# Performance work log

Measured on AMD Instinct MI355X. Metric: run time of the kernel, lower is better.

The kernel has to match this reference:

```python
import jax, jax.numpy as jnp
import numpy as np

B, L, H = 2, 1024, 768
DI, N, K, R = 1536, 16, 4, 48


def setup_inputs() -> dict:
    key = jax.random.key(0)
    ks = jax.random.split(key, 10)
    s = 0.02
    inp = {
        "x": jax.random.normal(ks[0], (B, L, H), jnp.float32),
        "in_up_w": jax.random.normal(ks[1], (2 * DI * 4, H), jnp.float32) * s,
        "in_down_w": jax.random.normal(ks[2], (2 * DI, 2 * DI * 4), jnp.float32) * s,
        "conv_w": jax.random.normal(ks[3], (DI, 1, K), jnp.float32) * 0.5,
        "conv_b": jnp.zeros((DI,), jnp.float32),
        "x_proj_w": jax.random.normal(ks[4], (R + 2 * N, DI), jnp.float32) * s,
        "dt_w": jax.random.normal(ks[5], (DI, R), jnp.float32) * s,
        "dt_b": jnp.full((DI,), -4.0, jnp.float32) + jax.random.normal(ks[6], (DI,), jnp.float32) * 0.1,
        "A_log": jnp.log(jnp.broadcast_to(jnp.arange(1, N + 1, dtype=jnp.float32)[None, :], (DI, N))),
        "D": jnp.ones((DI,), jnp.float32),
        "out_up_w": jax.random.normal(ks[7], (4 * DI, DI), jnp.float32) * s,
        "out_down_w": jax.random.normal(ks[8], (H, 4 * DI), jnp.float32) * s,
    }
    return inp


def reference(x, in_up_w, in_down_w, conv_w, conv_b, x_proj_w, dt_w, dt_b,
              A_log, D, out_up_w, out_down_w):
    act = jax.nn.silu
    # in_up_proj -> act -> in_down_proj  (use_bias=False)
    proj = act(x @ in_up_w.T) @ in_down_w.T          # [B, L, 2*DI]
    proj = proj.transpose(0, 2, 1)                   # [B, 2*DI, L]
    hs, gate = jnp.split(proj, 2, axis=1)            # each [B, DI, L]

    # depthwise causal conv1d (pad left K-1, truncate to L) + SiLU
    k = conv_w.shape[-1]
    c = hs.shape[1]
    y = jax.lax.conv_general_dilated(
        hs, conv_w, window_strides=(1,), padding=[(k - 1, 0)],
        feature_group_count=c, dimension_numbers=("NCH", "OIH", "NCH"))
    hs = act(y + conv_b[None, :, None])              # [B, DI, L]

    # x_proj -> split into dt / B / C
    ssm_p = jnp.einsum("bdl,kd->blk", hs, x_proj_w)  # [B, L, R+2N]
    r = dt_w.shape[1]
    n = A_log.shape[1]
    ts, Bm, Cm = jnp.split(ssm_p, [r, r + n], axis=-1)
    dt = jax.nn.softplus(ts @ dt_w.T + dt_b)         # [B, L, DI]
    dt = dt.transpose(0, 2, 1)                       # [B, DI, L]

    A = -jnp.exp(A_log)                              # [DI, N]
    dA = jnp.exp(dt[..., None] * A[None, :, None, :])        # [B, DI, L, N]
    dBu = dt[..., None] * Bm[:, None, :, :] * hs[..., None]  # [B, DI, L, N]

    def step(s, inps):
        dA_t, dBu_t, C_t = inps          # [B,DI,N], [B,DI,N], [B,N]
        s = dA_t * s + dBu_t
        return s, jnp.einsum("bdn,bn->bd", s, C_t)

    s0 = jnp.zeros((x.shape[0], c, n), x.dtype)
    _, ys = jax.lax.scan(
        step, s0,
        (dA.transpose(2, 0, 1, 3), dBu.transpose(2, 0, 1, 3), Cm.transpose(1, 0, 2)))
    yscan = ys.transpose(1, 2, 0)                    # [B, DI, L]

    yscan = yscan + hs * D[None, :, None]
    yscan = yscan * act(gate)

    # out_up_proj -> act -> out_down_proj (use_bias=False)
    out = act(yscan.transpose(0, 2, 1) @ out_up_w.T) @ out_down_w.T  # [B, L, H]
    return out
```

## Files before the change

### kernel.cpp

```cpp
#include <hip/hip_runtime.h>
#include <hip/hip_bf16.h>
#include <cstdint>

#define B_   2
#define L_   1024
#define H_   768
#define DI_  1536
#define DI2_ 3072
#define DUP_ 12288
#define DOUT_ 6144
#define N_   16
#define R_   48
#define SPW  128
#define BL_  2048
#define C_   64
#define CL_  16

typedef __bf16 bf16x8 __attribute__((ext_vector_type(8)));
typedef float  f32x4  __attribute__((ext_vector_type(4)));
typedef unsigned int u32;

__device__ __forceinline__ float silu_f(float v) {
    return v / (1.f + __expf(-v));
}

__device__ __forceinline__ void async_ld16(const void* g, void* lds) {
    __builtin_amdgcn_global_load_lds(
        (const __attribute__((address_space(1))) u32*)g,
        (__attribute__((address_space(3))) u32*)lds, 16, 0, 0);
}

__device__ __forceinline__ void cvt8(const float* __restrict__ s, __bf16* __restrict__ d, int i)
{
    const float4 a = *(const float4*)(s + i);
    const float4 b = *(const float4*)(s + i + 4);
    bf16x8 v;
    v[0] = (__bf16)a.x; v[1] = (__bf16)a.y; v[2] = (__bf16)a.z; v[3] = (__bf16)a.w;
    v[4] = (__bf16)b.x; v[5] = (__bf16)b.y; v[6] = (__bf16)b.z; v[7] = (__bf16)b.w;
    *(bf16x8*)(d + i) = v;
}

__global__ void prep1(const float* __restrict__ x, const float* __restrict__ wup,
                      const float* __restrict__ wdn,
                      __bf16* __restrict__ xb, __bf16* __restrict__ wupb,
                      __bf16* __restrict__ wdnb)
{
    const int bid = blockIdx.x;
    if (bid < 768)            cvt8(x,   xb,   (bid * 256 + threadIdx.x) * 8);
    else if (bid < 5376)      cvt8(wup, wupb, ((bid - 768) * 256 + threadIdx.x) * 8);
    else                      cvt8(wdn, wdnb, ((bid - 5376) * 256 + threadIdx.x) * 8);
}

__global__ void prep2(const float* __restrict__ woup, const float* __restrict__ wodn,
                      const float* __restrict__ xp, const float* __restrict__ dtw,
                      __bf16* __restrict__ woupb, __bf16* __restrict__ wodnb,
                      __bf16* __restrict__ xppad, float* __restrict__ dtwT)
{
    const int bid = blockIdx.x;
    if (bid < 4608)        cvt8(woup, woupb, (bid * 256 + threadIdx.x) * 8);
    else if (bid < 6912)   cvt8(wodn, wodnb, ((bid - 4608) * 256 + threadIdx.x) * 8);
    else if (bid < 7008) {
        const int i = ((bid - 6912) * 256 + threadIdx.x) * 8;
        const int j = i / DI_;
        bf16x8 v;
        if (j < 80) {
            const float4 a = *(const float4*)(xp + i);
            const float4 b = *(const float4*)(xp + i + 4);
            v[0] = (__bf16)a.x; v[1] = (__bf16)a.y; v[2] = (__bf16)a.z; v[3] = (__bf16)a.w;
            v[4] = (__bf16)b.x; v[5] = (__bf16)b.y; v[6] = (__bf16)b.z; v[7] = (__bf16)b.w;
        } else {
            for (int k = 0; k < 8; ++k) v[k] = (__bf16)0.f;
        }
        *(bf16x8*)(xppad + i) = v;
    } else {
        const int i = (bid - 7008) * 256 + threadIdx.x;
        const int r = i / DI_, d = i % DI_;
        dtwT[i] = dtw[(size_t)d * R_ + r];
    }
}

template<int EPI, int ATOMIC, typename OutT>
__global__ __launch_bounds__(256) void gemm_bf16(
    const __bf16* __restrict__ A, const __bf16* __restrict__ W, OutT* __restrict__ O,
    int M, int N, int Kslice, int lda, int ldw, int ldo)
{
    constexpr int BM = 128, BN = 128, BK = 32;
    __shared__ __bf16 As[BM * BK];
    __shared__ __bf16 Bs[BN * BK];

    const int tid  = threadIdx.x;
    const int bm   = blockIdx.x * BM;
    const int bn   = blockIdx.y * BN;
    const int kbase = blockIdx.z * Kslice;
    if (ATOMIC == 0) O += (size_t)blockIdx.z * (size_t)M * ldo;

    const int wave = tid >> 6, lane = tid & 63;
    const int wm = (wave >> 1) * 64, wn = (wave & 1) * 64;
    const int quad = lane >> 4, tr = lane & 15;

    const int srow = tid >> 2;
    const int skc  = ((tid & 3) ^ ((srow >> 1) & 3)) * 8;
    const __bf16* Ag0 = A + (size_t)(bm + srow) * lda + kbase + skc;
    const __bf16* Ag1 = A + (size_t)(bm + srow + 64) * lda + kbase + skc;
    const __bf16* Wg0 = W + (size_t)(bn + srow) * ldw + kbase + skc;
    const __bf16* Wg1 = W + (size_t)(bn + srow + 64) * ldw + kbase + skc;
    __bf16* Al0 = &As[tid * 8];
    __bf16* Al1 = &As[2048 + tid * 8];
    __bf16* Bl0 = &Bs[tid * 8];
    __bf16* Bl1 = &Bs[2048 + tid * 8];

    const int fsw = (quad ^ ((tr >> 1) & 3)) * 8;
    const __bf16* arp = &As[(wm + tr) * BK + fsw];
    const __bf16* brp = &Bs[(wn + tr) * BK + fsw];

    f32x4 acc[4][4];
#pragma unroll
    for (int i = 0; i < 4; ++i)
#pragma unroll
        for (int j = 0; j < 4; ++j) acc[i][j] = (f32x4){0.f, 0.f, 0.f, 0.f};

    for (int k0 = 0; k0 < Kslice; k0 += BK) {
        __syncthreads();
        async_ld16(Ag0 + k0, Al0);
        async_ld16(Ag1 + k0, Al1);
        async_ld16(Wg0 + k0, Bl0);
        async_ld16(Wg1 + k0, Bl1);
        __syncthreads();

        bf16x8 af[4], bfv[4];
#pragma unroll
        for (int i = 0; i < 4; ++i) af[i]  = *(const bf16x8*)(arp + i * 16 * BK);
#pragma unroll
        for (int j = 0; j < 4; ++j) bfv[j] = *(const bf16x8*)(brp + j * 16 * BK);
#pragma unroll
        for (int i = 0; i < 4; ++i)
#pragma unroll
            for (int j = 0; j < 4; ++j)
                acc[i][j] = __builtin_amdgcn_mfma_f32_16x16x32_bf16(af[i], bfv[j], acc[i][j], 0, 0, 0);
    }

#pragma unroll
    for (int i = 0; i < 4; ++i) {
        const int row = bm + wm + i * 16 + quad * 4;
#pragma unroll
        for (int j = 0; j < 4; ++j) {
            const int col = bn + wn + j * 16 + tr;
            OutT* op = O + (size_t)row * ldo + col;
#pragma unroll
            for (int r = 0; r < 4; ++r) {
                float v = acc[i][j][r];
                if (EPI == 1) v = silu_f(v);
                if (ATOMIC == 1) atomicAdd((float*)(op + (size_t)r * ldo), v);
                else             op[(size_t)r * ldo] = (OutT)v;
            }
        }
    }
}

__global__ void conv_kernel(const float* __restrict__ P0, const float* __restrict__ P1,
                            const float* __restrict__ cw, const float* __restrict__ cb,
                            float* __restrict__ HS, __bf16* __restrict__ HSb)
{
    const int t = blockIdx.x * blockDim.x + threadIdx.x;
    const int d = t % DI_;
    const int bl = t / DI_;
    const int l = bl % L_;
    const float4 w = *(const float4*)(cw + (size_t)d * 4);
    const float wk[4] = {w.x, w.y, w.z, w.w};
    float acc = cb[d];
#pragma unroll
    for (int k = 0; k < 4; ++k) {
        const int ls = l - 3 + k;
        if (ls >= 0) {
            const size_t idx = (size_t)(bl - l + ls) * DI2_ + d;
            acc += wk[k] * (P0[idx] + P1[idx]);
        }
    }
    const float h = silu_f(acc);
    HS[t]  = h;
    HSb[t] = (__bf16)h;
}

__global__ void dt_kernel(const float* __restrict__ SP, const float* __restrict__ dtwT,
                          const float* __restrict__ dtb, float* __restrict__ DT)
{
    const int t = blockIdx.x * blockDim.x + threadIdx.x;
    const int d = t % DI_;
    const int bl = t / DI_;
    const float* ts = SP + (size_t)bl * SPW;
    float s = dtb[d];
#pragma unroll
    for (int r4 = 0; r4 < R_ / 4; ++r4) {
        const float4 tv = *(const float4*)(ts + r4 * 4);
        const float* wp = dtwT + (size_t)r4 * 4 * DI_ + d;
        s += tv.x * wp[0] + tv.y * wp[DI_] + tv.z * wp[2 * DI_] + tv.w * wp[3 * DI_];
    }
    DT[t] = (s > 20.f) ? s : log1pf(__expf(s));
}

__global__ __launch_bounds__(256) void scan_pass1(
    const float* __restrict__ DT, const float* __restrict__ HS,
    const float* __restrict__ SP, const float* __restrict__ A_log,
    float* __restrict__ Aprod, float* __restrict__ Bacc)
{
    const int t = blockIdx.x * blockDim.x + threadIdx.x;
    const int d = t % DI_;
    const int y = t / DI_;
    const int c = y % C_;
    const int b = y / C_;
    float A[N_], s[N_], ap[N_];
    {
        const float4* alp = (const float4*)(A_log + (size_t)d * N_);
        const float4 a0 = alp[0], a1 = alp[1], a2 = alp[2], a3 = alp[3];
        const float av[N_] = {a0.x,a0.y,a0.z,a0.w, a1.x,a1.y,a1.z,a1.w,
                              a2.x,a2.y,a2.z,a2.w, a3.x,a3.y,a3.z,a3.w};
#pragma unroll
        for (int n = 0; n < N_; ++n) { A[n] = -__expf(av[n]); s[n] = 0.f; ap[n] = 1.f; }
    }
    for (int il = 0; il < CL_; ++il) {
        const size_t bl = (size_t)b * L_ + c * CL_ + il;
        const float dt = DT[bl * DI_ + d];
        const float hs = HS[bl * DI_ + d];
        const float4* Bp = (const float4*)(SP + bl * SPW + R_);
        const float4 b0 = Bp[0], b1 = Bp[1], b2 = Bp[2], b3 = Bp[3];
        const float Bv[N_] = {b0.x,b0.y,b0.z,b0.w, b1.x,b1.y,b1.z,b1.w,
                              b2.x,b2.y,b2.z,b2.w, b3.x,b3.y,b3.z,b3.w};
        const float dh = dt * hs;
#pragma unroll
        for (int n = 0; n < N_; ++n) {
            const float dA = __expf(dt * A[n]);
            s[n] = fmaf(dA, s[n], dh * Bv[n]);
            ap[n] *= dA;
        }
    }
    float4* Ap = (float4*)(Aprod + (size_t)t * N_);
    float4* Bc = (float4*)(Bacc  + (size_t)t * N_);
    Ap[0] = make_float4(ap[0], ap[1], ap[2], ap[3]);
    Ap[1] = make_float4(ap[4], ap[5], ap[6], ap[7]);
    Ap[2] = make_float4(ap[8], ap[9], ap[10], ap[11]);
    Ap[3] = make_float4(ap[12], ap[13], ap[14], ap[15]);
    Bc[0] = make_float4(s[0], s[1], s[2], s[3]);
    Bc[1] = make_float4(s[4], s[5], s[6], s[7]);
    Bc[2] = make_float4(s[8], s[9], s[10], s[11]);
    Bc[3] = make_float4(s[12], s[13], s[14], s[15]);
}

__global__ __launch_bounds__(256) void scan_pass2(
    const float* __restrict__ Aprod, const float* __restrict__ Bacc,
    float* __restrict__ Sinit)
{
    const int t = blockIdx.x * blockDim.x + threadIdx.x;
    const int n = t & (N_ - 1);
    const int d = (t >> 4) % DI_;
    const int b = (t >> 4) / DI_;
    float s = 0.f;
    for (int c = 0; c < C_; ++c) {
        const size_t idx = (((size_t)b * C_ + c) * DI_ + d) * N_ + n;
        Sinit[idx] = s;
        s = fmaf(Aprod[idx], s, Bacc[idx]);
    }
}

__global__ __launch_bounds__(256) void scan_pass3(
    const float* __restrict__ DT, const float* __restrict__ HS,
    const float* __restrict__ SP, const float* __restrict__ P0,
    const float* __restrict__ P1, const float* __restrict__ A_log,
    const float* __restrict__ Dv, const float* __restrict__ Sinit,
    __bf16* __restrict__ Y)
{
    const int t = blockIdx.x * blockDim.x + threadIdx.x;
    const int d = t % DI_;
    const int y = t / DI_;
    const int c = y % C_;
    const int b = y / C_;
    float A[N_], s[N_];
    {
        const float4* alp = (const float4*)(A_log + (size_t)d * N_);
        const float4 a0 = alp[0], a1 = alp[1], a2 = alp[2], a3 = alp[3];
        const float av[N_] = {a0.x,a0.y,a0.z,a0.w, a1.x,a1.y,a1.z,a1.w,
                              a2.x,a2.y,a2.z,a2.w, a3.x,a3.y,a3.z,a3.w};
#pragma unroll
        for (int n = 0; n < N_; ++n) A[n] = -__expf(av[n]);
    }
    {
        const float4* sp = (const float4*)(Sinit + (size_t)t * N_);
        const float4 s0 = sp[0], s1 = sp[1], s2 = sp[2], s3 = sp[3];
        s[0]=s0.x; s[1]=s0.y; s[2]=s0.z; s[3]=s0.w;
        s[4]=s1.x; s[5]=s1.y; s[6]=s1.z; s[7]=s1.w;
        s[8]=s2.x; s[9]=s2.y; s[10]=s2.z; s[11]=s2.w;
        s[12]=s3.x; s[13]=s3.y; s[14]=s3.z; s[15]=s3.w;
    }
    const float Dd = Dv[d];
    for (int il = 0; il < CL_; ++il) {
        const size_t bl = (size_t)b * L_ + c * CL_ + il;
        const float dt = DT[bl * DI_ + d];
        const float hs = HS[bl * DI_ + d];
        const float4* Bp = (const float4*)(SP + bl * SPW + R_);
        const float4 b0 = Bp[0], b1 = Bp[1], b2 = Bp[2], b3 = Bp[3];
        const float4 c0 = Bp[4], c1 = Bp[5], c2 = Bp[6], c3 = Bp[7];
        const float Bv[N_] = {b0.x,b0.y,b0.z,b0.w, b1.x,b1.y,b1.z,b1.w,
                              b2.x,b2.y,b2.z,b2.w, b3.x,b3.y,b3.z,b3.w};
        const float Cv[N_] = {c0.x,c0.y,c0.z,c0.w, c1.x,c1.y,c1.z,c1.w,
                              c2.x,c2.y,c2.z,c2.w, c3.x,c3.y,c3.z,c3.w};
        const float dh = dt * hs;
        float acc = 0.f;
#pragma unroll
        for (int n = 0; n < N_; ++n) {
            const float dA = __expf(dt * A[n]);
            s[n] = fmaf(dA, s[n], dh * Bv[n]);
            acc = fmaf(s[n], Cv[n], acc);
        }
        const size_t gidx = bl * DI2_ + DI_ + d;
        const float g = P0[gidx] + P1[gidx];
        Y[bl * DI_ + d] = (__bf16)((acc + hs * Dd) * silu_f(g));
    }
}

extern "C" void kernel_launch(void* const* d_in, const int* in_sizes, int n_in,
                              void* d_out, int out_size, void* d_ws, size_t ws_size,
                              hipStream_t stream) {
    const float* x        = (const float*)d_in[0];
    const float* w_up     = (const float*)d_in[1];
    const float* w_down   = (const float*)d_in[2];
    const float* conv_w   = (const float*)d_in[3];
    const float* conv_b   = (const float*)d_in[4];
    const float* x_proj_w = (const float*)d_in[5];
    const float* dt_w     = (const float*)d_in[6];
    const float* dt_b     = (const float*)d_in[7];
    const float* A_log    = (const float*)d_in[8];
    const float* Dvec     = (const float*)d_in[9];
    const float* w_oup    = (const float*)d_in[10];
    const float* w_odown  = (const float*)d_in[11];
    float* out = (float*)d_out;

    char* base = (char*)d_ws;
    __bf16* x_b      = (__bf16*)base;
    __bf16* wup_b    = (__bf16*)(base + 3145728);
    float*  P0       = (float*)base;
    float*  P1       = (float*)(base + 25165824);
    char* r2 = base + 50331648;
    __bf16* wdown_b  = (__bf16*)r2;
    __bf16* HSb      = (__bf16*)r2;
    float*  SPb      = (float*)(r2 + 6291456);
    float*  DTb      = (float*)(r2 + 7340032);
    __bf16* Yb       = (__bf16*)(r2 + 19922944);
    __bf16* XPpad    = (__bf16*)(r2 + 26214400);
    float*  dtwT     = (float*)(r2 + 26607616);
    __bf16* woup_b   = (__bf16*)(r2 + 26902528);
    __bf16* wodown_b = (__bf16*)(r2 + 45776896);
    char* r3 = r2 + 75497472;
    __bf16* U1b      = (__bf16*)r3;
    __bf16* U2b      = (__bf16*)r3;
    float*  Aprod    = (float*)r3;
    float*  Bacc     = (float*)(r3 + 12582912);
    float*  Sinit    = (float*)(r3 + 25165824);
    float*  HS       = (float*)(r3 + 37748736);

    prep1<<<23808, 256, 0, stream>>>(x, w_up, w_down, x_b, wup_b, wdown_b);

    gemm_bf16<1, 0, __bf16><<<dim3(16, 96, 1), 256, 0, stream>>>(
        x_b, wup_b, U1b, BL_, DUP_, H_, H_, H_, DUP_);

    gemm_bf16<0, 0, float><<<dim3(16, 24, 2), 256, 0, stream>>>(
        U1b, wdown_b, P0, BL_, DI2_, DUP_ / 2, DUP_, DUP_, DI2_);

    prep2<<<7296, 256, 0, stream>>>(w_oup, w_odown, x_proj_w, dt_w,
                                    woup_b, wodown_b, XPpad, dtwT);

    conv_kernel<<<(BL_ * DI_) / 256, 256, 0, stream>>>(P0, P1, conv_w, conv_b, HS, HSb);

    hipMemsetAsync(SPb, 0, (size_t)BL_ * SPW * 4, stream);
    gemm_bf16<0, 1, float><<<dim3(16, 1, 4), 256, 0, stream>>>(
        HSb, XPpad, SPb, BL_, SPW, DI_ / 4, DI_, DI_, SPW);

    dt_kernel<<<(BL_ * DI_) / 256, 256, 0, stream>>>(SPb, dtwT, dt_b, DTb);

    scan_pass1<<<(B_ * C_ * DI_) / 256, 256, 0, stream>>>(DTb, HS, SPb, A_log, Aprod, Bacc);
    scan_pass2<<<(B_ * DI_ * N_) / 256, 256, 0, stream>>>(Aprod, Bacc, Sinit);
    scan_pass3<<<(B_ * C_ * DI_) / 256, 256, 0, stream>>>(
        DTb, HS, SPb, P0, P1, A_log, Dvec, Sinit, Yb);

    gemm_bf16<1, 0, __bf16><<<dim3(16, 48, 1), 256, 0, stream>>>(
        Yb, woup_b, U2b, BL_, DOUT_, DI_, DI_, DI_, DOUT_);

    hipMemsetAsync(out, 0, (size_t)BL_ * H_ * 4, stream);
    gemm_bf16<0, 1, float><<<dim3(16, 6, 8), 256, 0, stream>>>(
        U2b, wodown_b, out, BL_, H_, DOUT_ / 8, DOUT_, DOUT_, H_);
}
```

Measured before the change: 825.2 us.

## Replace atomic split-K with partial buffers and reductions, swizzle blocks, drop fp32 HS

The two atomic split-K GEMMs (x_proj and out_down) now write per-slice partial outputs, which small reduce kernels then sum. This removes the memsets and the atomic traffic. The x_proj split grows from 4 to 8 slices and out_down shrinks from 8 to 4. The down-projection GEMM gets a block-index swizzle to improve cache locality. The fp32 copy of the conv output is dropped, so the scan passes read the bf16 version instead, cutting memory traffic at a small cost in precision.

```diff
diff --git a/kernel.cpp b/kernel.cpp
--- a/kernel.cpp
+++ b/kernel.cpp
@@ -79,7 +79,7 @@
     }
 }
 
-template<int EPI, int ATOMIC, typename OutT>
+template<int EPI, int ATOMIC, int SWZ, typename OutT>
 __global__ __launch_bounds__(256) void gemm_bf16(
     const __bf16* __restrict__ A, const __bf16* __restrict__ W, OutT* __restrict__ O,
     int M, int N, int Kslice, int lda, int ldw, int ldo)
@@ -89,8 +89,16 @@
     __shared__ __bf16 Bs[BN * BK];
 
     const int tid  = threadIdx.x;
-    const int bm   = blockIdx.x * BM;
-    const int bn   = blockIdx.y * BN;
+    int bx = blockIdx.x, by = blockIdx.y;
+    if (SWZ) {
+        const int nxy  = gridDim.x * gridDim.y;
+        const int flat = blockIdx.x + gridDim.x * blockIdx.y;
+        const int qq   = nxy >> 3;
+        const int s    = (flat & 7) * qq + (flat >> 3);
+        bx = s % gridDim.x; by = s / gridDim.x;
+    }
+    const int bm   = bx * BM;
+    const int bn   = by * BN;
     const int kbase = blockIdx.z * Kslice;
     if (ATOMIC == 0) O += (size_t)blockIdx.z * (size_t)M * ldo;
 
@@ -157,9 +165,33 @@
     }
 }
 
+__global__ void reduce_sp(const float* __restrict__ SPp, float* __restrict__ SPb)
+{
+    const int i = (blockIdx.x * 256 + threadIdx.x) * 4;
+    float4 a = *(const float4*)(SPp + i);
+#pragma unroll
+    for (int z = 1; z < 8; ++z) {
+        const float4 b = *(const float4*)(SPp + (size_t)z * (BL_ * SPW) + i);
+        a.x += b.x; a.y += b.y; a.z += b.z; a.w += b.w;
+    }
+    *(float4*)(SPb + i) = a;
+}
+
+__global__ void reduce_out(const float* __restrict__ OP, float* __restrict__ out)
+{
+    const int i = (blockIdx.x * 256 + threadIdx.x) * 4;
+    float4 a = *(const float4*)(OP + i);
+#pragma unroll
+    for (int z = 1; z < 4; ++z) {
+        const float4 b = *(const float4*)(OP + (size_t)z * (BL_ * H_) + i);
+        a.x += b.x; a.y += b.y; a.z += b.z; a.w += b.w;
+    }
+    *(float4*)(out + i) = a;
+}
+
 __global__ void conv_kernel(const float* __restrict__ P0, const float* __restrict__ P1,
                             const float* __restrict__ cw, const float* __restrict__ cb,
-                            float* __restrict__ HS, __bf16* __restrict__ HSb)
+                            __bf16* __restrict__ HSb)
 {
     const int t = blockIdx.x * blockDim.x + threadIdx.x;
     const int d = t % DI_;
@@ -176,9 +208,7 @@
             acc += wk[k] * (P0[idx] + P1[idx]);
         }
     }
-    const float h = silu_f(acc);
-    HS[t]  = h;
-    HSb[t] = (__bf16)h;
+    HSb[t] = (__bf16)silu_f(acc);
 }
 
 __global__ void dt_kernel(const float* __restrict__ SP, const float* __restrict__ dtwT,
@@ -199,7 +229,7 @@
 }
 
 __global__ __launch_bounds__(256) void scan_pass1(
-    const float* __restrict__ DT, const float* __restrict__ HS,
+    const float* __restrict__ DT, const __bf16* __restrict__ HSb,
     const float* __restrict__ SP, const float* __restrict__ A_log,
     float* __restrict__ Aprod, float* __restrict__ Bacc)
 {
@@ -220,7 +250,7 @@
     for (int il = 0; il < CL_; ++il) {
         const size_t bl = (size_t)b * L_ + c * CL_ + il;
         const float dt = DT[bl * DI_ + d];
-        const float hs = HS[bl * DI_ + d];
+        const float hs = (float)HSb[bl * DI_ + d];
         const float4* Bp = (const float4*)(SP + bl * SPW + R_);
         const float4 b0 = Bp[0], b1 = Bp[1], b2 = Bp[2], b3 = Bp[3];
         const float Bv[N_] = {b0.x,b0.y,b0.z,b0.w, b1.x,b1.y,b1.z,b1.w,
@@ -262,7 +292,7 @@
 }
 
 __global__ __launch_bounds__(256) void scan_pass3(
-    const float* __restrict__ DT, const float* __restrict__ HS,
+    const float* __restrict__ DT, const __bf16* __restrict__ HSb,
     const float* __restrict__ SP, const float* __restrict__ P0,
     const float* __restrict__ P1, const float* __restrict__ A_log,
     const float* __restrict__ Dv, const float* __restrict__ Sinit,
@@ -294,7 +324,7 @@
     for (int il = 0; il < CL_; ++il) {
         const size_t bl = (size_t)b * L_ + c * CL_ + il;
         const float dt = DT[bl * DI_ + d];
-        const float hs = HS[bl * DI_ + d];
+        const float hs = (float)HSb[bl * DI_ + d];
         const float4* Bp = (const float4*)(SP + bl * SPW + R_);
         const float4 b0 = Bp[0], b1 = Bp[1], b2 = Bp[2], b3 = Bp[3];
         const float4 c0 = Bp[4], c1 = Bp[5], c2 = Bp[6], c3 = Bp[7];
@@ -342,48 +372,49 @@
     __bf16* wdown_b  = (__bf16*)r2;
     __bf16* HSb      = (__bf16*)r2;
     float*  SPb      = (float*)(r2 + 6291456);
-    float*  DTb      = (float*)(r2 + 7340032);
-    __bf16* Yb       = (__bf16*)(r2 + 19922944);
-    __bf16* XPpad    = (__bf16*)(r2 + 26214400);
-    float*  dtwT     = (float*)(r2 + 26607616);
-    __bf16* woup_b   = (__bf16*)(r2 + 26902528);
-    __bf16* wodown_b = (__bf16*)(r2 + 45776896);
+    float*  SPp      = (float*)(r2 + 7340032);
+    float*  DTb      = (float*)(r2 + 15728640);
+    __bf16* Yb       = (__bf16*)(r2 + 28311552);
+    __bf16* XPpad    = (__bf16*)(r2 + 34603008);
+    float*  dtwT     = (float*)(r2 + 34996224);
+    __bf16* woup_b   = (__bf16*)(r2 + 35291136);
+    __bf16* wodown_b = (__bf16*)(r2 + 54165504);
     char* r3 = r2 + 75497472;
     __bf16* U1b      = (__bf16*)r3;
     __bf16* U2b      = (__bf16*)r3;
     float*  Aprod    = (float*)r3;
     float*  Bacc     = (float*)(r3 + 12582912);
     float*  Sinit    = (float*)(r3 + 25165824);
-    float*  HS       = (float*)(r3 + 37748736);
+    float*  OP       = (float*)(r3 + 25165824);
 
     prep1<<<23808, 256, 0, stream>>>(x, w_up, w_down, x_b, wup_b, wdown_b);
 
-    gemm_bf16<1, 0, __bf16><<<dim3(16, 96, 1), 256, 0, stream>>>(
+    gemm_bf16<1, 0, 0, __bf16><<<dim3(16, 96, 1), 256, 0, stream>>>(
         x_b, wup_b, U1b, BL_, DUP_, H_, H_, H_, DUP_);
 
-    gemm_bf16<0, 0, float><<<dim3(16, 24, 2), 256, 0, stream>>>(
+    gemm_bf16<0, 0, 1, float><<<dim3(16, 24, 2), 256, 0, stream>>>(
         U1b, wdown_b, P0, BL_, DI2_, DUP_ / 2, DUP_, DUP_, DI2_);
 
     prep2<<<7296, 256, 0, stream>>>(w_oup, w_odown, x_proj_w, dt_w,
                                     woup_b, wodown_b, XPpad, dtwT);
 
-    conv_kernel<<<(BL_ * DI_) / 256, 256, 0, stream>>>(P0, P1, conv_w, conv_b, HS, HSb);
-
-    hipMemsetAsync(SPb, 0, (size_t)BL_ * SPW * 4, stream);
-    gemm_bf16<0, 1, float><<<dim3(16, 1, 4), 256, 0, stream>>>(
-        HSb, XPpad, SPb, BL_, SPW, DI_ / 4, DI_, DI_, SPW);
+    conv_kernel<<<(BL_ * DI_) / 256, 256, 0, stream>>>(P0, P1, conv_w, conv_b, HSb);
+
+    gemm_bf16<0, 0, 0, float><<<dim3(16, 1, 8), 256, 0, stream>>>(
+        HSb, XPpad, SPp, BL_, SPW, DI_ / 8, DI_, DI_, SPW);
+    reduce_sp<<<(BL_ * SPW) / 1024, 256, 0, stream>>>(SPp, SPb);
 
     dt_kernel<<<(BL_ * DI_) / 256, 256, 0, stream>>>(SPb, dtwT, dt_b, DTb);
 
-    scan_pass1<<<(B_ * C_ * DI_) / 256, 256, 0, stream>>>(DTb, HS, SPb, A_log, Aprod, Bacc);
+    scan_pass1<<<(B_ * C_ * DI_) / 256, 256, 0, stream>>>(DTb, HSb, SPb, A_log, Aprod, Bacc);
     scan_pass2<<<(B_ * DI_ * N_) / 256, 256, 0, stream>>>(Aprod, Bacc, Sinit);
     scan_pass3<<<(B_ * C_ * DI_) / 256, 256, 0, stream>>>(
-        DTb, HS, SPb, P0, P1, A_log, Dvec, Sinit, Yb);
-
-    gemm_bf16<1, 0, __bf16><<<dim3(16, 48, 1), 256, 0, stream>>>(
+        DTb, HSb, SPb, P0, P1, A_log, Dvec, Sinit, Yb);
+
+    gemm_bf16<1, 0, 0, __bf16><<<dim3(16, 48, 1), 256, 0, stream>>>(
         Yb, woup_b, U2b, BL_, DOUT_, DI_, DI_, DI_, DOUT_);
 
-    hipMemsetAsync(out, 0, (size_t)BL_ * H_ * 4, stream);
-    gemm_bf16<0, 1, float><<<dim3(16, 6, 8), 256, 0, stream>>>(
-        U2b, wodown_b, out, BL_, H_, DOUT_ / 8, DOUT_, DOUT_, H_);
-}
+    gemm_bf16<0, 0, 0, float><<<dim3(16, 6, 4), 256, 0, stream>>>(
+        U2b, wodown_b, OP, BL_, H_, DOUT_ / 4, DOUT_, DOUT_, H_);
+    reduce_out<<<(BL_ * H_) / 1024, 256, 0, stream>>>(OP, out);
+}
```

New measurement: 820.9 us. Within noise of the previous version (-0.5%).
